# Performance work log

Measured on AMD Instinct MI355X. Metric: run time of the kernel, lower is better.

## Reference

```python
import jax, jax.numpy as jnp
import numpy as np

NPROJS = 128
SPACING = 4.7952
MU0 = 0.013


def setup_inputs() -> dict:
    key = jax.random.key(0)
    B, P, L, S = 1, NPROJS, 1024, 256
    projs = jax.random.uniform(key, (B, P, L, S), dtype=jnp.float32)
    return {"projs": projs}


def reference(projs):
    # Faithful to the torch module: edcc is reset to None at the start of every
    # i-iteration, so the returned value is determined solely by the LAST
    # iteration i=127, j=(127+30)%128=29, accumulated over all l rows.
    B, P, L, S = projs.shape
    theta = jnp.linspace(0.0, 2.0 * jnp.pi, NPROJS + 1)[:-1]
    i, j = NPROJS - 1, (NPROJS - 1 + 30) % NPROJS  # 127, 29
    sigma = MU0 * jnp.tan((theta[i] - theta[j]) / 2.0)
    # Laplace-transform weights: s grid centered at 0, step = SPACING
    s = jnp.linspace((-S * SPACING + SPACING) / 2.0,
                     (S * SPACING - SPACING) / 2.0, S)
    exp_s = jnp.exp(sigma * s * SPACING).astype(projs.dtype)  # [S]
    # Vectorized Laplace transform across all l rows at once: [B, L]
    P_i = jnp.einsum('bls,s->bl', projs[:, i], exp_s)
    P_j = jnp.einsum('bls,s->bl', projs[:, j], exp_s)
    den = P_i + P_j
    term = jnp.where(den != 0,
                     (2.0 / NPROJS) * jnp.abs(P_i - P_j) / den,
                     jnp.zeros_like(den))
    edcc = term.sum(axis=1)  # accumulate over l -> [B]
    return edcc.mean()
```

## Files before the change

### kernel.cpp

```cpp
#include <hip/hip_runtime.h>
#include <math.h>


#define NPROJS   128
#define L_ROWS   1024
#define S_LEN    256
#define I_ROW    127
#define J_ROW    29

__global__ __launch_bounds__(256) void edcc_kernel(const float* __restrict__ projs,
                                                   float* __restrict__ out) {
    const int gwave = (blockIdx.x * blockDim.x + threadIdx.x) >> 6;
    const int lane  = threadIdx.x & 63;
    if (gwave >= L_ROWS) return;
    const int l = gwave;

    const double sigma = 0.013 * tan((98.0 * (6.283185307179586 / 128.0)) * 0.5);

    const float* rowi = projs + ((size_t)(I_ROW * L_ROWS + l)) * S_LEN;
    const float* rowj = projs + ((size_t)(J_ROW * L_ROWS + l)) * S_LEN;

    const float4 vi = *reinterpret_cast<const float4*>(rowi + lane * 4);
    const float4 vj = *reinterpret_cast<const float4*>(rowj + lane * 4);
    const float ai[4] = {vi.x, vi.y, vi.z, vi.w};
    const float bj[4] = {vj.x, vj.y, vj.z, vj.w};

    float pi_sum = 0.0f, pj_sum = 0.0f;
#pragma unroll
    for (int c = 0; c < 4; ++c) {
        const int k = lane * 4 + c;
        const double s_k = ((double)k - 127.5) * 4.7952;
        const float  w   = expf((float)(sigma * s_k * 4.7952));
        pi_sum = fmaf(ai[c], w, pi_sum);
        pj_sum = fmaf(bj[c], w, pj_sum);
    }

#pragma unroll
    for (int off = 32; off > 0; off >>= 1) {
        pi_sum += __shfl_xor(pi_sum, off);
        pj_sum += __shfl_xor(pj_sum, off);
    }

    if (lane == 0) {
        const float den  = pi_sum + pj_sum;
        const float term = (den != 0.0f)
                             ? (2.0f / (float)NPROJS) * fabsf(pi_sum - pj_sum) / den
                             : 0.0f;
        atomicAdd(out, term);
    }
}

extern "C" void kernel_launch(void* const* d_in, const int* in_sizes, int n_in,
                              void* d_out, int out_size, void* d_ws, size_t ws_size,
                              hipStream_t stream) {
    const float* projs = (const float*)d_in[0];
    float* out = (float*)d_out;

    hipMemsetAsync(out, 0, sizeof(float) * (size_t)out_size, stream);

    const int threads = 256;
    const int blocks  = (L_ROWS * 64) / threads;
    edcc_kernel<<<blocks, threads, 0, stream>>>(projs, out);
}
```

Before: 169.1 us.

## Process four rows per wave and reduce per block before one atomic

Each wave now handles four L rows instead of one, with the exp weights computed once per lane and reused across rows. Per-wave results are summed through shared memory so each of 16 blocks issues a single atomicAdd, replacing 1024 contended atomics. The grid shrinks from 256 blocks to 16 blocks of 1024 threads, which uses far fewer CUs and could reduce memory-level parallelism for the 2 MB read.

```diff
diff --git a/kernel.cpp b/kernel.cpp
--- a/kernel.cpp
+++ b/kernel.cpp
@@ -2,51 +2,57 @@
 #include <math.h>
 
 
-#define NPROJS   128
 #define L_ROWS   1024
 #define S_LEN    256
 #define I_ROW    127
 #define J_ROW    29
+#define THREADS  1024
+#define BLOCKS   16
 
-__global__ __launch_bounds__(256) void edcc_kernel(const float* __restrict__ projs,
-                                                   float* __restrict__ out) {
-    const int gwave = (blockIdx.x * blockDim.x + threadIdx.x) >> 6;
-    const int lane  = threadIdx.x & 63;
-    if (gwave >= L_ROWS) return;
-    const int l = gwave;
+__global__ __launch_bounds__(THREADS) void edcc_kernel(const float* __restrict__ projs,
+                                                       float* __restrict__ out) {
+    const int wid  = threadIdx.x >> 6;
+    const int lane = threadIdx.x & 63;
+    const int gw   = blockIdx.x * (THREADS / 64) + wid;
 
     const double sigma = 0.013 * tan((98.0 * (6.283185307179586 / 128.0)) * 0.5);
-
-    const float* rowi = projs + ((size_t)(I_ROW * L_ROWS + l)) * S_LEN;
-    const float* rowj = projs + ((size_t)(J_ROW * L_ROWS + l)) * S_LEN;
-
-    const float4 vi = *reinterpret_cast<const float4*>(rowi + lane * 4);
-    const float4 vj = *reinterpret_cast<const float4*>(rowj + lane * 4);
-    const float ai[4] = {vi.x, vi.y, vi.z, vi.w};
-    const float bj[4] = {vj.x, vj.y, vj.z, vj.w};
-
-    float pi_sum = 0.0f, pj_sum = 0.0f;
+    float w[4];
 #pragma unroll
     for (int c = 0; c < 4; ++c) {
-        const int k = lane * 4 + c;
-        const double s_k = ((double)k - 127.5) * 4.7952;
-        const float  w   = expf((float)(sigma * s_k * 4.7952));
-        pi_sum = fmaf(ai[c], w, pi_sum);
-        pj_sum = fmaf(bj[c], w, pj_sum);
+        const double s_k = ((double)(lane * 4 + c) - 127.5) * 4.7952;
+        w[c] = expf((float)(sigma * s_k * 4.7952));
     }
 
+    float term_sum = 0.0f;
 #pragma unroll
-    for (int off = 32; off > 0; off >>= 1) {
-        pi_sum += __shfl_xor(pi_sum, off);
-        pj_sum += __shfl_xor(pj_sum, off);
+    for (int r = 0; r < 4; ++r) {
+        const int l = gw + 256 * r;
+        const float* rowi = projs + ((size_t)(I_ROW * L_ROWS + l)) * S_LEN;
+        const float* rowj = projs + ((size_t)(J_ROW * L_ROWS + l)) * S_LEN;
+        const float4 vi = *reinterpret_cast<const float4*>(rowi + lane * 4);
+        const float4 vj = *reinterpret_cast<const float4*>(rowj + lane * 4);
+
+        float pi = fmaf(vi.x, w[0], fmaf(vi.y, w[1], fmaf(vi.z, w[2], vi.w * w[3])));
+        float pj = fmaf(vj.x, w[0], fmaf(vj.y, w[1], fmaf(vj.z, w[2], vj.w * w[3])));
+
+#pragma unroll
+        for (int off = 32; off > 0; off >>= 1) {
+            pi += __shfl_xor(pi, off);
+            pj += __shfl_xor(pj, off);
+        }
+        const float den = pi + pj;
+        if (den != 0.0f)
+            term_sum += (2.0f / 128.0f) * fabsf(pi - pj) / den;
     }
 
-    if (lane == 0) {
-        const float den  = pi_sum + pj_sum;
-        const float term = (den != 0.0f)
-                             ? (2.0f / (float)NPROJS) * fabsf(pi_sum - pj_sum) / den
-                             : 0.0f;
-        atomicAdd(out, term);
+    __shared__ float lds[THREADS / 64];
+    if (lane == 0) lds[wid] = term_sum;
+    __syncthreads();
+    if (wid == 0) {
+        float v = (lane < THREADS / 64) ? lds[lane] : 0.0f;
+#pragma unroll
+        for (int off = 32; off > 0; off >>= 1) v += __shfl_xor(v, off);
+        if (lane == 0) atomicAdd(out, v);
     }
 }
 
@@ -58,7 +64,5 @@
 
     hipMemsetAsync(out, 0, sizeof(float) * (size_t)out_size, stream);
 
-    const int threads = 256;
-    const int blocks  = (L_ROWS * 64) / threads;
-    edcc_kernel<<<blocks, threads, 0, stream>>>(projs, out);
+    edcc_kernel<<<BLOCKS, THREADS, 0, stream>>>(projs, out);
 }
```

New measurement: 159.3 us. -5.8%, faster.
